# Kernel tuning notes

Hardware: AMD Instinct MI355X
Metric: run time of the kernel (lower is better)

Reference implementation:

```python
import jax, jax.numpy as jnp
import numpy as np

S, B, D, H, L = 1024, 2, 1024, 16, 4
HD = D // H            # 64
MLP = 4 * D            # 4096
EPS = 1e-5


def _ln(x, w, b):
    m = x.mean(-1, keepdims=True)
    v = ((x - m) ** 2).mean(-1, keepdims=True)
    return (x - m) * jax.lax.rsqrt(v + EPS) * w + b


def _rotate_half(x):
    h = x.shape[-1] // 2
    return jnp.concatenate([-x[..., h:], x[..., :h]], axis=-1)


def _rope(t, cos, sin):
    # t: (B, S, H, HD); cos/sin: (S, HD) broadcast to (1, S, 1, HD)
    return t * cos[None, :, None, :] + _rotate_half(t) * sin[None, :, None, :]


def setup_inputs() -> dict:
    key = jax.random.key(0)
    ks = iter(jax.random.split(key, 64))

    def p(shape, scale=0.02):
        return jax.random.normal(next(ks), shape, jnp.float32) * scale

    return {
        "x": jax.random.normal(next(ks), (S, B, D), jnp.float32),
        "rotary_pos_emb": jax.random.normal(next(ks), (S, HD // 2), jnp.float32),
        # stacked per-layer params (leading dim L) for lax.scan
        "ln1_w": jnp.ones((L, D), jnp.float32), "ln1_b": jnp.zeros((L, D), jnp.float32),
        "in_w": p((L, 3 * D, D)), "in_b": jnp.zeros((L, 3 * D), jnp.float32),
        "out_w": p((L, D, D)), "out_b": jnp.zeros((L, D), jnp.float32),
        "ln2_w": jnp.ones((L, D), jnp.float32), "ln2_b": jnp.zeros((L, D), jnp.float32),
        "fc_w": p((L, MLP, D)), "fc_b": jnp.zeros((L, MLP), jnp.float32),
        "cp_w": p((L, D, MLP)), "cp_b": jnp.zeros((L, D), jnp.float32),
        # attention pooling head (qkv_bias=False in CrossAttention)
        "pn_q_w": jnp.ones((D,), jnp.float32), "pn_q_b": jnp.zeros((D,), jnp.float32),
        "pn_k_w": jnp.ones((D,), jnp.float32), "pn_k_b": jnp.zeros((D,), jnp.float32),
        "pn_v_w": jnp.ones((D,), jnp.float32), "pn_v_b": jnp.zeros((D,), jnp.float32),
        "pq_w": p((D, D)), "pk_w": p((D, D)), "pv_w": p((D, D)),
        "pp_w": p((D, D)), "pp_b": jnp.zeros((D,), jnp.float32),
    }


def reference(x, rotary_pos_emb, ln1_w, ln1_b, in_w, in_b, out_w, out_b,
              ln2_w, ln2_b, fc_w, fc_b, cp_w, cp_b,
              pn_q_w, pn_q_b, pn_k_w, pn_k_b, pn_v_w, pn_v_b,
              pq_w, pk_w, pv_w, pp_w, pp_b):
    # freqs (S, HD/2) -> cos/sin tiled twice along last dim: (S, HD)
    cos = jnp.tile(jnp.cos(rotary_pos_emb), (1, 2))
    sin = jnp.tile(jnp.sin(rotary_pos_emb), (1, 2))
    scale = 1.0 / np.sqrt(HD).astype(np.float32)

    def layer(h, p):
        l1w, l1b, iw, ib, ow, ob, l2w, l2b, fw, fb, cw, cb = p
        a = _ln(h, l1w, l1b)
        qkv = jnp.einsum('sbd,ed->sbe', a, iw) + ib           # (S,B,3D)
        qkv = qkv.reshape(S, B, 3, H, HD)
        q = jnp.transpose(qkv[:, :, 0], (1, 0, 2, 3))          # (B,S,H,HD)
        k = jnp.transpose(qkv[:, :, 1], (1, 0, 2, 3))
        v = jnp.transpose(qkv[:, :, 2], (1, 0, 2, 3))
        q = _rope(q, cos, sin)
        k = _rope(k, cos, sin)
        q, k, v = (t.transpose(0, 2, 1, 3) for t in (q, k, v))  # (B,H,S,HD)
        attn = jax.nn.softmax(jnp.einsum('bhsd,bhtd->bhst', q, k) * scale, axis=-1)
        o = jnp.einsum('bhst,bhtd->bhsd', attn, v)
        o = o.transpose(2, 0, 1, 3).reshape(S, B, D)           # back to (S,B,D)
        h = h + jnp.einsum('sbd,ed->sbe', o, ow) + ob          # residual + out_proj
        m = _ln(h, l2w, l2b)
        m = jax.nn.gelu(jnp.einsum('sbd,ed->sbe', m, fw) + fb, approximate=False)
        h = h + jnp.einsum('sbe,de->sbd', m, cw) + cb          # residual + c_proj
        return h, None

    h, _ = jax.lax.scan(layer, x, (ln1_w, ln1_b, in_w, in_b, out_w, out_b,
                                   ln2_w, ln2_b, fc_w, fc_b, cp_w, cp_b))

    # AttentionPoolingBlock: mean-pooled single query, cross-attend over tokens
    t = h.transpose(1, 0, 2)                                   # (B,N,C)
    xq = _ln(t.mean(1, keepdims=True), pn_q_w, pn_q_b)         # (B,1,C)
    xk = _ln(t, pn_k_w, pn_k_b)
    xv = _ln(t, pn_v_w, pn_v_b)
    q = (xq @ pq_w.T).reshape(B, 1, H, HD).transpose(0, 2, 1, 3)   # (B,H,1,HD)
    k = (xk @ pk_w.T).reshape(B, S, H, HD).transpose(0, 2, 1, 3)
    v = (xv @ pv_w.T).reshape(B, S, H, HD).transpose(0, 2, 1, 3)
    a = jax.nn.softmax(jnp.einsum('bhqd,bhtd->bhqt', q, k) * scale, axis=-1)
    o = jnp.einsum('bhqt,bhtd->bhqd', a, v).transpose(0, 2, 1, 3).reshape(B, 1, D)
    return (o @ pp_w.T + pp_b)[:, 0]                           # (B, D)
```

## Files before the change

### kernel.cpp

```cpp
#include <hip/hip_runtime.h>
#include <math.h>

#define S_LEN  1024
#define BATCH  2
#define DMODEL 1024
#define NHEAD  16
#define HDIM   64
#define NLAYER 4
#define MLPD   4096
#define MROWS  (S_LEN*BATCH)

typedef __attribute__((ext_vector_type(8))) short bf16x8_t;
typedef __attribute__((ext_vector_type(4))) float f32x4_t;

__device__ __forceinline__ unsigned short f2bf(float f) {
  union { float f; unsigned u; } c; c.f = f;
  return (unsigned short)((c.u + 0x7FFFu + ((c.u >> 16) & 1u)) >> 16);
}
__device__ __forceinline__ float bf2f(unsigned short u) {
  union { unsigned u; float f; } c; c.u = ((unsigned)u) << 16; return c.f;
}

__device__ __forceinline__ void gl_lds16(const unsigned short* g, unsigned short* l) {
  __builtin_amdgcn_global_load_lds(
      (const __attribute__((address_space(1))) unsigned int*)(g),
      (__attribute__((address_space(3))) unsigned int*)(l), 16, 0, 0);
}

__global__ __launch_bounds__(256) void w2bf_kernel(const float* __restrict__ src,
    unsigned short* __restrict__ dst, int n) {
  const int i = (blockIdx.x * 256 + threadIdx.x) * 8;
  if (i >= n) return;
  float4 v0 = *(const float4*)(src + i);
  float4 v1 = *(const float4*)(src + i + 4);
  ushort4 u0, u1;
  u0.x = f2bf(v0.x); u0.y = f2bf(v0.y); u0.z = f2bf(v0.z); u0.w = f2bf(v0.w);
  u1.x = f2bf(v1.x); u1.y = f2bf(v1.y); u1.z = f2bf(v1.z); u1.w = f2bf(v1.w);
  *(ushort4*)(dst + i)     = u0;
  *(ushort4*)(dst + i + 4) = u1;
}

template<bool BF16OUT>
__global__ __launch_bounds__(256) void ln_kernel(const float* __restrict__ x,
    const float* __restrict__ w, const float* __restrict__ b,
    void* __restrict__ out, float inscale) {
  const int row = blockIdx.x;
  const int tid = threadIdx.x;
  const float* xr = x + (size_t)row * DMODEL;
  float4 v = *(const float4*)(xr + tid * 4);
  v.x *= inscale; v.y *= inscale; v.z *= inscale; v.w *= inscale;
  float s1 = v.x + v.y + v.z + v.w;
  float s2 = v.x*v.x + v.y*v.y + v.z*v.z + v.w*v.w;
  #pragma unroll
  for (int off = 32; off; off >>= 1) {
    s1 += __shfl_xor(s1, off);
    s2 += __shfl_xor(s2, off);
  }
  __shared__ float as1[4], as2[4];
  if ((tid & 63) == 0) { as1[tid >> 6] = s1; as2[tid >> 6] = s2; }
  __syncthreads();
  s1 = as1[0] + as1[1] + as1[2] + as1[3];
  s2 = as2[0] + as2[1] + as2[2] + as2[3];
  const float mean = s1 * (1.0f / DMODEL);
  const float var  = s2 * (1.0f / DMODEL) - mean * mean;
  const float r = rsqrtf(var + 1e-5f);
  float4 wv = *(const float4*)(w + tid * 4);
  float4 bv = *(const float4*)(b + tid * 4);
  float o0 = (v.x - mean) * r * wv.x + bv.x;
  float o1 = (v.y - mean) * r * wv.y + bv.y;
  float o2 = (v.z - mean) * r * wv.z + bv.z;
  float o3 = (v.w - mean) * r * wv.w + bv.w;
  if (BF16OUT) {
    ushort4 u; u.x = f2bf(o0); u.y = f2bf(o1); u.z = f2bf(o2); u.w = f2bf(o3);
    *(ushort4*)((unsigned short*)out + (size_t)row * DMODEL + tid * 4) = u;
  } else {
    float4 ov; ov.x = o0; ov.y = o1; ov.z = o2; ov.w = o3;
    *(float4*)((float*)out + (size_t)row * DMODEL + tid * 4) = ov;
  }
}

template<int SPLIT, bool GELU, bool ATOMIC, bool OUTBF16>
__global__ __launch_bounds__(256, 3) void gemm_mfma(
    const unsigned short* __restrict__ A, const unsigned short* __restrict__ W,
    const float* __restrict__ bias, void* __restrict__ Cout,
    int M, int N, int K) {
  constexpr int BK = 32;
  __shared__ __align__(16) unsigned short As[2][128 * BK];
  __shared__ __align__(16) unsigned short Bs[2][128 * BK];
  const int tid  = threadIdx.x;
  const int wid  = tid >> 6;
  const int lane = tid & 63;
  const int lrow = lane & 15;
  const int lq   = lane >> 4;

  const int NB = gridDim.x, MB = gridDim.y;
  const int f = blockIdx.y * NB + blockIdx.x;
  const int xcd = f & 7;
  const int idx = f >> 3;
  const int m0 = (idx % MB) * 128;
  const int n0 = (xcd + (idx / MB) * 8) * 128;

  const int wm = (wid >> 1) * 64;
  const int wn = (wid & 1) * 64;
  const int Kc = K / SPLIT;
  const int kbase = blockIdx.z * Kc;

  f32x4_t acc[4][4];
  #pragma unroll
  for (int i = 0; i < 4; ++i)
    #pragma unroll
    for (int j = 0; j < 4; ++j) acc[i][j] = (f32x4_t){0.f, 0.f, 0.f, 0.f};

  const int c1 = tid, c2 = tid + 256;
  const unsigned short* Ag1 = A + (size_t)(m0 + (c1 >> 2)) * K + kbase + (c1 & 3) * 8;
  const unsigned short* Ag2 = A + (size_t)(m0 + (c2 >> 2)) * K + kbase + (c2 & 3) * 8;
  const unsigned short* Wg1 = W + (size_t)(n0 + (c1 >> 2)) * K + kbase + (c1 & 3) * 8;
  const unsigned short* Wg2 = W + (size_t)(n0 + (c2 >> 2)) * K + kbase + (c2 & 3) * 8;
  const int l1 = c1 * 8, l2 = c2 * 8;

  gl_lds16(Ag1, &As[0][l1]);
  gl_lds16(Ag2, &As[0][l2]);
  gl_lds16(Wg1, &Bs[0][l1]);
  gl_lds16(Wg2, &Bs[0][l2]);
  __syncthreads();

  int cur = 0;
  for (int k0 = 0; k0 < Kc; k0 += BK) {
    if (k0 + BK < Kc) {
      gl_lds16(Ag1 + k0 + BK, &As[cur ^ 1][l1]);
      gl_lds16(Ag2 + k0 + BK, &As[cur ^ 1][l2]);
      gl_lds16(Wg1 + k0 + BK, &Bs[cur ^ 1][l1]);
      gl_lds16(Wg2 + k0 + BK, &Bs[cur ^ 1][l2]);
    }

    bf16x8_t af[4], bfr[4];
    #pragma unroll
    for (int i = 0; i < 4; ++i)
      af[i] = *(const bf16x8_t*)&As[cur][(wm + i * 16 + lrow) * BK + lq * 8];
    #pragma unroll
    for (int j = 0; j < 4; ++j)
      bfr[j] = *(const bf16x8_t*)&Bs[cur][(wn + j * 16 + lrow) * BK + lq * 8];
    #pragma unroll
    for (int i = 0; i < 4; ++i)
      #pragma unroll
      for (int j = 0; j < 4; ++j)
        acc[i][j] = __builtin_amdgcn_mfma_f32_16x16x32_bf16(af[i], bfr[j], acc[i][j], 0, 0, 0);

    __syncthreads();
    cur ^= 1;
  }

  float bj[4];
  #pragma unroll
  for (int j = 0; j < 4; ++j)
    bj[j] = (bias && (SPLIT == 1 || blockIdx.z == 0)) ? bias[n0 + wn + j * 16 + lrow] : 0.f;
  #pragma unroll
  for (int i = 0; i < 4; ++i) {
    #pragma unroll
    for (int r = 0; r < 4; ++r) {
      const int row = m0 + wm + i * 16 + lq * 4 + r;
      const size_t idx2 = (size_t)row * N + n0 + wn + lrow;
      #pragma unroll
      for (int j = 0; j < 4; ++j) {
        float val = acc[i][j][r] + bj[j];
        if (GELU)
          val = 0.5f * val * (1.0f + erff(val * 0.70710678118654752f));
        if (ATOMIC)
          atomicAdd(&((float*)Cout)[idx2 + j * 16], val);
        else if (OUTBF16)
          ((unsigned short*)Cout)[idx2 + j * 16] = f2bf(val);
        else
          ((float*)Cout)[idx2 + j * 16] = val;
      }
    }
  }
}

__global__ __launch_bounds__(256) void rope_kernel(const unsigned short* __restrict__ qkv,
    const float* __restrict__ rot, unsigned short* __restrict__ qt,
    unsigned short* __restrict__ kt, unsigned short* __restrict__ vt) {
  const int idx = blockIdx.x * 256 + threadIdx.x;
  const int d  = idx & 63;
  const int hh = (idx >> 6) & 15;
  const int m  = idx >> 10;
  const int s  = m >> 1;
  const int b  = m & 1;
  const float f  = rot[s * 32 + (d & 31)];
  const float cs = cosf(f);
  const float sn = sinf(f);
  const float sign = (d < 32) ? -1.0f : 1.0f;
  const size_t base  = (size_t)m * 3072 + hh * 64;
  const int bh = b * 16 + hh;
  const size_t obase = (((size_t)bh * 1024 + s) << 6) + d;
  float qv = bf2f(qkv[base + d]);
  float qp = bf2f(qkv[base + (d ^ 32)]);
  qt[obase] = f2bf(qv * cs + sign * qp * sn);
  float kv = bf2f(qkv[base + 1024 + d]);
  float kp = bf2f(qkv[base + 1024 + (d ^ 32)]);
  kt[obase] = f2bf(kv * cs + sign * kp * sn);
  vt[(((size_t)bh * 64 + d) << 10) + s] = qkv[base + 2048 + d];
}

__global__ __launch_bounds__(256, 2) void attn_kernel(
    const unsigned short* __restrict__ q, const unsigned short* __restrict__ k,
    const unsigned short* __restrict__ vtr, unsigned short* __restrict__ o) {
  const int tid  = threadIdx.x;
  const int wid  = tid >> 6;
  const int lane = tid & 63;
  const int col  = lane & 15;
  const int quad = lane >> 4;
  const int bh   = blockIdx.x >> 4;
  const int qw   = (blockIdx.x & 15) * 64 + wid * 16;

  __shared__ __align__(16) unsigned short Ks[64 * 72];
  __shared__ __align__(16) unsigned short Vs[64 * 72];
  __shared__ __align__(16) unsigned short Pl_[4][16 * 72];
  unsigned short* Pl = Pl_[wid];

  const unsigned short* kb = k   + ((size_t)bh << 16);
  const unsigned short* vb = vtr + ((size_t)bh << 16);

  bf16x8_t qa0, qa1;
  {
    const unsigned short* qp = q + ((((size_t)bh << 10) + qw + col) << 6) + quad * 8;
    qa0 = *(const bf16x8_t*)(qp);
    qa1 = *(const bf16x8_t*)(qp + 32);
  }

  f32x4_t oacc[4];
  #pragma unroll
  for (int j = 0; j < 4; ++j) oacc[j] = (f32x4_t){0.f, 0.f, 0.f, 0.f};
  float mr[4] = {-3.0e38f, -3.0e38f, -3.0e38f, -3.0e38f};
  float lr[4] = {0.f, 0.f, 0.f, 0.f};

  const int srow = tid >> 2;
  const int scol = (tid & 3) * 16;

  for (int t0 = 0; t0 < 1024; t0 += 64) {
    __syncthreads();
    {
      const unsigned short* gk = kb + (size_t)(t0 + srow) * 64 + scol;
      const unsigned short* gv = vb + (size_t)srow * 1024 + t0 + scol;
      uint4 ka = *(const uint4*)(gk);
      uint4 kc = *(const uint4*)(gk + 8);
      uint4 va = *(const uint4*)(gv);
      uint4 vc = *(const uint4*)(gv + 8);
      *(uint4*)&Ks[srow * 72 + scol]     = ka;
      *(uint4*)&Ks[srow * 72 + scol + 8] = kc;
      *(uint4*)&Vs[srow * 72 + scol]     = va;
      *(uint4*)&Vs[srow * 72 + scol + 8] = vc;
    }
    __syncthreads();

    f32x4_t sc[4];
    #pragma unroll
    for (int j = 0; j < 4; ++j) {
      bf16x8_t kf0 = *(const bf16x8_t*)&Ks[(j * 16 + col) * 72 + quad * 8];
      bf16x8_t kf1 = *(const bf16x8_t*)&Ks[(j * 16 + col) * 72 + quad * 8 + 32];
      f32x4_t c = (f32x4_t){0.f, 0.f, 0.f, 0.f};
      c = __builtin_amdgcn_mfma_f32_16x16x32_bf16(qa0, kf0, c, 0, 0, 0);
      c = __builtin_amdgcn_mfma_f32_16x16x32_bf16(qa1, kf1, c, 0, 0, 0);
      sc[j] = c;
    }

    #pragma unroll
    for (int r = 0; r < 4; ++r) {
      float s0 = sc[0][r] * 0.125f, s1 = sc[1][r] * 0.125f;
      float s2 = sc[2][r] * 0.125f, s3 = sc[3][r] * 0.125f;
      float rm = fmaxf(fmaxf(s0, s1), fmaxf(s2, s3));
      rm = fmaxf(rm, __shfl_xor(rm, 1));
      rm = fmaxf(rm, __shfl_xor(rm, 2));
      rm = fmaxf(rm, __shfl_xor(rm, 4));
      rm = fmaxf(rm, __shfl_xor(rm, 8));
      const float mn = fmaxf(mr[r], rm);
      const float alpha = __expf(mr[r] - mn);
      mr[r] = mn;
      const float p0 = __expf(s0 - mn), p1 = __expf(s1 - mn);
      const float p2 = __expf(s2 - mn), p3 = __expf(s3 - mn);
      float rs = p0 + p1 + p2 + p3;
      rs += __shfl_xor(rs, 1);
      rs += __shfl_xor(rs, 2);
      rs += __shfl_xor(rs, 4);
      rs += __shfl_xor(rs, 8);
      lr[r] = lr[r] * alpha + rs;
      #pragma unroll
      for (int j = 0; j < 4; ++j) oacc[j][r] *= alpha;
      const int prow = (quad * 4 + r) * 72;
      Pl[prow +  0 + col] = f2bf(p0);
      Pl[prow + 16 + col] = f2bf(p1);
      Pl[prow + 32 + col] = f2bf(p2);
      Pl[prow + 48 + col] = f2bf(p3);
    }

    bf16x8_t pa0 = *(const bf16x8_t*)&Pl[col * 72 + quad * 8];
    bf16x8_t pa1 = *(const bf16x8_t*)&Pl[col * 72 + quad * 8 + 32];
    #pragma unroll
    for (int j = 0; j < 4; ++j) {
      bf16x8_t vf0 = *(const bf16x8_t*)&Vs[(j * 16 + col) * 72 + quad * 8];
      bf16x8_t vf1 = *(const bf16x8_t*)&Vs[(j * 16 + col) * 72 + quad * 8 + 32];
      oacc[j] = __builtin_amdgcn_mfma_f32_16x16x32_bf16(pa0, vf0, oacc[j], 0, 0, 0);
      oacc[j] = __builtin_amdgcn_mfma_f32_16x16x32_bf16(pa1, vf1, oacc[j], 0, 0, 0);
    }
  }

  const int b = bh >> 4, hh = bh & 15;
  #pragma unroll
  for (int r = 0; r < 4; ++r) {
    const float inv = 1.0f / lr[r];
    const int sq = qw + quad * 4 + r;
    unsigned short* orow = o + (((size_t)sq * 2 + b) << 10) + hh * 64;
    #pragma unroll
    for (int j = 0; j < 4; ++j)
      orow[j * 16 + col] = f2bf(oacc[j][r] * inv);
  }
}

__global__ __launch_bounds__(256) void mean_kernel(const float* __restrict__ h,
    float* __restrict__ tsum) {
  const int idx = blockIdx.x * 256 + threadIdx.x;
  const int bd = idx & 2047;
  const int sc = idx >> 11;
  const int b = bd >> 10, d = bd & 1023;
  float sm = 0.f;
  for (int s = sc * 128; s < sc * 128 + 128; ++s)
    sm += h[(((size_t)s * 2 + b) << 10) + d];
  atomicAdd(&tsum[bd], sm);
}

__global__ __launch_bounds__(256) void smallmv_kernel(const float* __restrict__ in,
    const float* __restrict__ W, const float* __restrict__ bias,
    float* __restrict__ out) {
  const int lane = threadIdx.x & 63;
  const int n = blockIdx.x * 4 + (threadIdx.x >> 6);
  const int b = blockIdx.y;
  const float* wr = W + (size_t)n * 1024;
  const float* xr = in + (size_t)b * 1024;
  float sm = 0.f;
  #pragma unroll
  for (int j = 0; j < 4; ++j) {
    float4 wv = *(const float4*)(wr + lane * 4 + j * 256);
    float4 xv = *(const float4*)(xr + lane * 4 + j * 256);
    sm += wv.x * xv.x + wv.y * xv.y + wv.z * xv.z + wv.w * xv.w;
  }
  #pragma unroll
  for (int off = 32; off; off >>= 1) sm += __shfl_xor(sm, off);
  if (lane == 0) out[(size_t)b * 1024 + n] = sm + (bias ? bias[n] : 0.f);
}

__global__ __launch_bounds__(256) void pool_attn_part(const float* __restrict__ q,
    const float* __restrict__ k, const float* __restrict__ v,
    float* __restrict__ part) {
  const int wid  = (blockIdx.x * 256 + threadIdx.x) >> 6;
  const int lane = threadIdx.x & 63;
  const int bh = wid >> 4, kblk = wid & 15;
  const int b = bh >> 4, hh = bh & 15;
  const float qd = q[(size_t)b * 1024 + hh * 64 + lane];
  float mx = -3.0e38f, l = 0.f, acc = 0.f;
  for (int t = kblk * 64; t < kblk * 64 + 64; ++t) {
    const size_t ro = (((size_t)t * 2 + b) << 10) + hh * 64 + lane;
    float p = qd * k[ro];
    p += __shfl_xor(p, 32); p += __shfl_xor(p, 16); p += __shfl_xor(p, 8);
    p += __shfl_xor(p, 4);  p += __shfl_xor(p, 2);  p += __shfl_xor(p, 1);
    const float sc = p * 0.125f;
    const float mn = fmaxf(mx, sc);
    const float alpha = __expf(mx - mn);
    const float w = __expf(sc - mn);
    acc = acc * alpha + w * v[ro];
    l   = l * alpha + w;
    mx  = mn;
  }
  float* pp = part + (size_t)wid * 68;
  if (lane == 0) { pp[0] = mx; pp[1] = l; }
  pp[4 + lane] = acc;
}

__global__ __launch_bounds__(256) void pool_attn_comb(const float* __restrict__ part,
    float* __restrict__ o) {
  const int wid  = (blockIdx.x * 256 + threadIdx.x) >> 6;
  const int lane = threadIdx.x & 63;
  const float* pb = part + (size_t)wid * 16 * 68;
  float M = -3.0e38f;
  #pragma unroll
  for (int w = 0; w < 16; ++w) M = fmaxf(M, pb[w * 68]);
  float L = 0.f, O = 0.f;
  #pragma unroll
  for (int w = 0; w < 16; ++w) {
    const float e = __expf(pb[w * 68] - M);
    L += e * pb[w * 68 + 1];
    O += e * pb[w * 68 + 4 + lane];
  }
  const int b = wid >> 4, hh = wid & 15;
  o[(size_t)b * 1024 + hh * 64 + lane] = O / L;
}

extern "C" void kernel_launch(void* const* d_in, const int* in_sizes, int n_in,
                              void* d_out, int out_size, void* d_ws, size_t ws_size,
                              hipStream_t stream) {
  (void)in_sizes; (void)n_in; (void)out_size; (void)ws_size;
  const float* x     = (const float*)d_in[0];
  const float* rot   = (const float*)d_in[1];
  const float* ln1_w = (const float*)d_in[2];
  const float* ln1_b = (const float*)d_in[3];
  const float* in_w  = (const float*)d_in[4];
  const float* in_b  = (const float*)d_in[5];
  const float* out_w = (const float*)d_in[6];
  const float* out_b = (const float*)d_in[7];
  const float* ln2_w = (const float*)d_in[8];
  const float* ln2_b = (const float*)d_in[9];
  const float* fc_w  = (const float*)d_in[10];
  const float* fc_b  = (const float*)d_in[11];
  const float* cp_w  = (const float*)d_in[12];
  const float* cp_b  = (const float*)d_in[13];
  const float* pn_q_w = (const float*)d_in[14];
  const float* pn_q_b = (const float*)d_in[15];
  const float* pn_k_w = (const float*)d_in[16];
  const float* pn_k_b = (const float*)d_in[17];
  const float* pn_v_w = (const float*)d_in[18];
  const float* pn_v_b = (const float*)d_in[19];
  const float* pq_w  = (const float*)d_in[20];
  const float* pk_w  = (const float*)d_in[21];
  const float* pv_w  = (const float*)d_in[22];
  const float* pp_w  = (const float*)d_in[23];
  const float* pp_b  = (const float*)d_in[24];

  float* ws = (float*)d_ws;
  const size_t M1 = 1u << 20;
  float* h  = ws;
  float* a  = ws + 2 * M1;
  float* r1 = ws + 4 * M1;
  float* qt = ws + 12 * M1;
  float* kt = ws + 14 * M1;
  float* vt = ws + 16 * M1;
  float* o  = ws + 18 * M1;
  float* wbf = ws + 20 * M1;
  unsigned short* a_bf  = (unsigned short*)a;
  unsigned short* r1_bf = (unsigned short*)r1;
  unsigned short* o_bf  = (unsigned short*)o;
  unsigned short* qt_bf = (unsigned short*)qt;
  unsigned short* kt_bf = (unsigned short*)kt;
  unsigned short* vt_bf = (unsigned short*)vt;
  unsigned short* wb_qkv = (unsigned short*)wbf;
  unsigned short* wb_out = wb_qkv + 3145728;
  unsigned short* wb_fc  = wb_out + 1048576;
  unsigned short* wb_cp  = wb_fc  + 4194304;
  float* tsum  = qt;
  float* xq    = qt + 2048;
  float* qpool = qt + 4096;
  float* opool = qt + 6144;
  float* ppart = qt + 8192;

  hipMemcpyAsync(h, x, 2 * M1 * sizeof(float), hipMemcpyDeviceToDevice, stream);

  for (int l = 0; l < NLAYER; ++l) {
    w2bf_kernel<<<3145728 / 2048, 256, 0, stream>>>(in_w + (size_t)l * 3145728, wb_qkv, 3145728);
    w2bf_kernel<<<1048576 / 2048, 256, 0, stream>>>(out_w + (size_t)l * 1048576, wb_out, 1048576);
    w2bf_kernel<<<4194304 / 2048, 256, 0, stream>>>(fc_w + (size_t)l * 4194304, wb_fc, 4194304);
    w2bf_kernel<<<4194304 / 2048, 256, 0, stream>>>(cp_w + (size_t)l * 4194304, wb_cp, 4194304);

    ln_kernel<true><<<MROWS, 256, 0, stream>>>(h, ln1_w + l * DMODEL, ln1_b + l * DMODEL, a_bf, 1.0f);
    gemm_mfma<1, false, false, true><<<dim3(3072 / 128, MROWS / 128, 1), 256, 0, stream>>>(
        a_bf, wb_qkv, in_b + l * 3072, r1_bf, MROWS, 3072, 1024);
    rope_kernel<<<8192, 256, 0, stream>>>(r1_bf, rot, qt_bf, kt_bf, vt_bf);
    attn_kernel<<<512, 256, 0, stream>>>(qt_bf, kt_bf, vt_bf, o_bf);
    gemm_mfma<4, false, true, false><<<dim3(1024 / 128, MROWS / 128, 4), 256, 0, stream>>>(
        o_bf, wb_out, out_b + l * 1024, h, MROWS, 1024, 1024);
    ln_kernel<true><<<MROWS, 256, 0, stream>>>(h, ln2_w + l * DMODEL, ln2_b + l * DMODEL, a_bf, 1.0f);
    gemm_mfma<1, true, false, true><<<dim3(4096 / 128, MROWS / 128, 1), 256, 0, stream>>>(
        a_bf, wb_fc, fc_b + l * 4096, r1_bf, MROWS, 4096, 1024);
    gemm_mfma<4, false, true, false><<<dim3(1024 / 128, MROWS / 128, 4), 256, 0, stream>>>(
        r1_bf, wb_cp, cp_b + l * 1024, h, MROWS, 1024, 4096);
  }

  hipMemsetAsync(tsum, 0, 2048 * sizeof(float), stream);
  mean_kernel<<<64, 256, 0, stream>>>(h, tsum);
  ln_kernel<false><<<BATCH, 256, 0, stream>>>(tsum, pn_q_w, pn_q_b, xq, 1.0f / S_LEN);
  ln_kernel<true><<<MROWS, 256, 0, stream>>>(h, pn_k_w, pn_k_b, a_bf, 1.0f);
  ln_kernel<true><<<MROWS, 256, 0, stream>>>(h, pn_v_w, pn_v_b, r1_bf, 1.0f);
  smallmv_kernel<<<dim3(256, BATCH), 256, 0, stream>>>(xq, pq_w, nullptr, qpool);
  w2bf_kernel<<<1048576 / 2048, 256, 0, stream>>>(pk_w, wb_qkv, 1048576);
  w2bf_kernel<<<1048576 / 2048, 256, 0, stream>>>(pv_w, wb_out, 1048576);
  hipMemsetAsync(kt, 0, (size_t)MROWS * DMODEL * sizeof(float), stream);
  hipMemsetAsync(vt, 0, (size_t)MROWS * DMODEL * sizeof(float), stream);
  gemm_mfma<4, false, true, false><<<dim3(1024 / 128, MROWS / 128, 4), 256, 0, stream>>>(
      a_bf, wb_qkv, nullptr, kt, MROWS, 1024, 1024);
  gemm_mfma<4, false, true, false><<<dim3(1024 / 128, MROWS / 128, 4), 256, 0, stream>>>(
      r1_bf, wb_out, nullptr, vt, MROWS, 1024, 1024);
  pool_attn_part<<<128, 256, 0, stream>>>(qpool, kt, vt, ppart);
  pool_attn_comb<<<8, 256, 0, stream>>>(ppart, opool);
  smallmv_kernel<<<dim3(256, BATCH), 256, 0, stream>>>(opool, pp_w, pp_b, (float*)d_out);
}
```

Baseline: 1.245 ms.

## Replace atomic split-K accumulation with partial buffers and fused reduce+LayerNorm

Split-K GEMMs for out_proj, c_proj and the pooling K/V projections now write per-split partial tiles to scratch buffers instead of doing float atomicAdd into the destination. A new reduce kernel sums the partials, adds bias and the residual, and optionally applies the following LayerNorm to emit bf16 activations, which removes the standalone LN launches and the memsets. The pooling projections drop from split 4 to split 2. This trades atomic contention for extra partial-buffer write and read traffic and relies on the reused workspace regions not overlapping.

```diff
diff --git a/kernel.cpp b/kernel.cpp
--- a/kernel.cpp
+++ b/kernel.cpp
@@ -79,7 +79,55 @@
   }
 }
 
-template<int SPLIT, bool GELU, bool ATOMIC, bool OUTBF16>
+template<int NS, bool ADDDEST, bool DOLN>
+__global__ __launch_bounds__(256) void reduce_ln_kernel(
+    const float* __restrict__ part, const float* __restrict__ bias,
+    float* __restrict__ dest, const float* __restrict__ lnw,
+    const float* __restrict__ lnb, unsigned short* __restrict__ lnout) {
+  const int row = blockIdx.x;
+  const int tid = threadIdx.x;
+  const size_t off = (size_t)row * DMODEL + tid * 4;
+  float4 v;
+  if (ADDDEST) v = *(const float4*)(dest + off);
+  else { v.x = 0.f; v.y = 0.f; v.z = 0.f; v.w = 0.f; }
+  if (bias) {
+    float4 b4 = *(const float4*)(bias + tid * 4);
+    v.x += b4.x; v.y += b4.y; v.z += b4.z; v.w += b4.w;
+  }
+  #pragma unroll
+  for (int z = 0; z < NS; ++z) {
+    float4 p = *(const float4*)(part + (size_t)z * (MROWS * DMODEL) + off);
+    v.x += p.x; v.y += p.y; v.z += p.z; v.w += p.w;
+  }
+  *(float4*)(dest + off) = v;
+  if (DOLN) {
+    float s1 = v.x + v.y + v.z + v.w;
+    float s2 = v.x*v.x + v.y*v.y + v.z*v.z + v.w*v.w;
+    #pragma unroll
+    for (int o = 32; o; o >>= 1) {
+      s1 += __shfl_xor(s1, o);
+      s2 += __shfl_xor(s2, o);
+    }
+    __shared__ float as1[4], as2[4];
+    if ((tid & 63) == 0) { as1[tid >> 6] = s1; as2[tid >> 6] = s2; }
+    __syncthreads();
+    s1 = as1[0] + as1[1] + as1[2] + as1[3];
+    s2 = as2[0] + as2[1] + as2[2] + as2[3];
+    const float mean = s1 * (1.0f / DMODEL);
+    const float var  = s2 * (1.0f / DMODEL) - mean * mean;
+    const float r = rsqrtf(var + 1e-5f);
+    float4 wv = *(const float4*)(lnw + tid * 4);
+    float4 bv = *(const float4*)(lnb + tid * 4);
+    ushort4 u;
+    u.x = f2bf((v.x - mean) * r * wv.x + bv.x);
+    u.y = f2bf((v.y - mean) * r * wv.y + bv.y);
+    u.z = f2bf((v.z - mean) * r * wv.z + bv.z);
+    u.w = f2bf((v.w - mean) * r * wv.w + bv.w);
+    *(ushort4*)(lnout + (size_t)row * DMODEL + tid * 4) = u;
+  }
+}
+
+template<int SPLIT, bool GELU, bool PARTIAL, bool OUTBF16>
 __global__ __launch_bounds__(256, 3) void gemm_mfma(
     const unsigned short* __restrict__ A, const unsigned short* __restrict__ W,
     const float* __restrict__ bias, void* __restrict__ Cout,
@@ -150,6 +198,7 @@
     cur ^= 1;
   }
 
+  const size_t zoff = PARTIAL ? (size_t)blockIdx.z * ((size_t)M * N) : 0;
   float bj[4];
   #pragma unroll
   for (int j = 0; j < 4; ++j)
@@ -165,8 +214,8 @@
         float val = acc[i][j][r] + bj[j];
         if (GELU)
           val = 0.5f * val * (1.0f + erff(val * 0.70710678118654752f));
-        if (ATOMIC)
-          atomicAdd(&((float*)Cout)[idx2 + j * 16], val);
+        if (PARTIAL)
+          ((float*)Cout)[zoff + idx2 + j * 16] = val;
         else if (OUTBF16)
           ((unsigned short*)Cout)[idx2 + j * 16] = f2bf(val);
         else
@@ -443,6 +492,9 @@
   unsigned short* wb_out = wb_qkv + 3145728;
   unsigned short* wb_fc  = wb_out + 1048576;
   unsigned short* wb_cp  = wb_fc  + 4194304;
+  float* part_op = r1;
+  float* part_cp = qt;
+  float* part_pool = ws + 5 * M1;
   float* tsum  = qt;
   float* xq    = qt + 2048;
   float* qpool = qt + 4096;
@@ -451,24 +503,33 @@
 
   hipMemcpyAsync(h, x, 2 * M1 * sizeof(float), hipMemcpyDeviceToDevice, stream);
 
+  ln_kernel<true><<<MROWS, 256, 0, stream>>>(h, ln1_w, ln1_b, a_bf, 1.0f);
+
   for (int l = 0; l < NLAYER; ++l) {
     w2bf_kernel<<<3145728 / 2048, 256, 0, stream>>>(in_w + (size_t)l * 3145728, wb_qkv, 3145728);
     w2bf_kernel<<<1048576 / 2048, 256, 0, stream>>>(out_w + (size_t)l * 1048576, wb_out, 1048576);
     w2bf_kernel<<<4194304 / 2048, 256, 0, stream>>>(fc_w + (size_t)l * 4194304, wb_fc, 4194304);
     w2bf_kernel<<<4194304 / 2048, 256, 0, stream>>>(cp_w + (size_t)l * 4194304, wb_cp, 4194304);
 
-    ln_kernel<true><<<MROWS, 256, 0, stream>>>(h, ln1_w + l * DMODEL, ln1_b + l * DMODEL, a_bf, 1.0f);
     gemm_mfma<1, false, false, true><<<dim3(3072 / 128, MROWS / 128, 1), 256, 0, stream>>>(
         a_bf, wb_qkv, in_b + l * 3072, r1_bf, MROWS, 3072, 1024);
     rope_kernel<<<8192, 256, 0, stream>>>(r1_bf, rot, qt_bf, kt_bf, vt_bf);
     attn_kernel<<<512, 256, 0, stream>>>(qt_bf, kt_bf, vt_bf, o_bf);
     gemm_mfma<4, false, true, false><<<dim3(1024 / 128, MROWS / 128, 4), 256, 0, stream>>>(
-        o_bf, wb_out, out_b + l * 1024, h, MROWS, 1024, 1024);
-    ln_kernel<true><<<MROWS, 256, 0, stream>>>(h, ln2_w + l * DMODEL, ln2_b + l * DMODEL, a_bf, 1.0f);
+        o_bf, wb_out, nullptr, part_op, MROWS, 1024, 1024);
+    reduce_ln_kernel<4, true, true><<<MROWS, 256, 0, stream>>>(
+        part_op, out_b + l * 1024, h, ln2_w + l * DMODEL, ln2_b + l * DMODEL, a_bf);
     gemm_mfma<1, true, false, true><<<dim3(4096 / 128, MROWS / 128, 1), 256, 0, stream>>>(
         a_bf, wb_fc, fc_b + l * 4096, r1_bf, MROWS, 4096, 1024);
     gemm_mfma<4, false, true, false><<<dim3(1024 / 128, MROWS / 128, 4), 256, 0, stream>>>(
-        r1_bf, wb_cp, cp_b + l * 1024, h, MROWS, 1024, 4096);
+        r1_bf, wb_cp, nullptr, part_cp, MROWS, 1024, 4096);
+    if (l < NLAYER - 1)
+      reduce_ln_kernel<4, true, true><<<MROWS, 256, 0, stream>>>(
+          part_cp, cp_b + l * 1024, h,
+          ln1_w + (l + 1) * DMODEL, ln1_b + (l + 1) * DMODEL, a_bf);
+    else
+      reduce_ln_kernel<4, true, false><<<MROWS, 256, 0, stream>>>(
+          part_cp, cp_b + l * 1024, h, nullptr, nullptr, nullptr);
   }
 
   hipMemsetAsync(tsum, 0, 2048 * sizeof(float), stream);
@@ -479,12 +540,14 @@
   smallmv_kernel<<<dim3(256, BATCH), 256, 0, stream>>>(xq, pq_w, nullptr, qpool);
   w2bf_kernel<<<1048576 / 2048, 256, 0, stream>>>(pk_w, wb_qkv, 1048576);
   w2bf_kernel<<<1048576 / 2048, 256, 0, stream>>>(pv_w, wb_out, 1048576);
-  hipMemsetAsync(kt, 0, (size_t)MROWS * DMODEL * sizeof(float), stream);
-  hipMemsetAsync(vt, 0, (size_t)MROWS * DMODEL * sizeof(float), stream);
-  gemm_mfma<4, false, true, false><<<dim3(1024 / 128, MROWS / 128, 4), 256, 0, stream>>>(
-      a_bf, wb_qkv, nullptr, kt, MROWS, 1024, 1024);
-  gemm_mfma<4, false, true, false><<<dim3(1024 / 128, MROWS / 128, 4), 256, 0, stream>>>(
-      r1_bf, wb_out, nullptr, vt, MROWS, 1024, 1024);
+  gemm_mfma<2, false, true, false><<<dim3(1024 / 128, MROWS / 128, 2), 256, 0, stream>>>(
+      a_bf, wb_qkv, nullptr, part_pool, MROWS, 1024, 1024);
+  reduce_ln_kernel<2, false, false><<<MROWS, 256, 0, stream>>>(
+      part_pool, nullptr, kt, nullptr, nullptr, nullptr);
+  gemm_mfma<2, false, true, false><<<dim3(1024 / 128, MROWS / 128, 2), 256, 0, stream>>>(
+      r1_bf, wb_out, nullptr, part_pool, MROWS, 1024, 1024);
+  reduce_ln_kernel<2, false, false><<<MROWS, 256, 0, stream>>>(
+      part_pool, nullptr, vt, nullptr, nullptr, nullptr);
   pool_attn_part<<<128, 256, 0, stream>>>(qpool, kt, vt, ppart);
   pool_attn_comb<<<8, 256, 0, stream>>>(ppart, opool);
   smallmv_kernel<<<dim3(256, BATCH), 256, 0, stream>>>(opool, pp_w, pp_b, (float*)d_out);
```

New measurement: 1.102 ms. -11.5%, faster.
